# Performance work log

Measured on AMD Instinct MI355X. Metric: run time of the kernel, lower is better.

The kernel has to match this reference:

```python
import jax, jax.numpy as jnp
import numpy as np
from jax import lax

B, T, DE, DT = 64, 511, 400, 100
D = DE + DT              # encoder + tag embedding concat
S = T + 1                # head sentinel prepended
HG, HE, M = 384, 64, 32  # graph hidden, edge hidden, band width


def lstm_layer(x, h0, c0, Wih, Whh, bih, bhh):
    """x: [N, L, in] -> [N, L, H]; torch LSTM gate order (i, f, g, o)."""
    def step(carry, xt):
        h, c = carry
        gates = xt @ Wih.T + bih + h @ Whh.T + bhh
        i, f, g, o = jnp.split(gates, 4, axis=-1)
        c = jax.nn.sigmoid(f) * c + jax.nn.sigmoid(i) * jnp.tanh(g)
        h = jax.nn.sigmoid(o) * jnp.tanh(c)
        return (h, c), h
    _, ys = lax.scan(step, (h0, c0), jnp.swapaxes(x, 0, 1))
    return jnp.swapaxes(ys, 0, 1)


def setup_inputs() -> dict:
    key = jax.random.key(0)
    ks = jax.random.split(key, 32)
    def u(k, shape, h):
        s = 1.0 / np.sqrt(h)
        return jax.random.uniform(k, shape, jnp.float32, -s, s)
    return {
        "input": jax.random.normal(ks[0], (B, T, DE), jnp.float32),
        "tag_embeddings": jax.random.normal(ks[1], (B, T, DT), jnp.float32),
        "mask": jnp.ones((B, T), jnp.int32),
        "head_indices": jax.random.randint(ks[2], (B, T), 0, S),
        "head_sentinel": jax.random.normal(ks[3], (D,), jnp.float32),
        "bos_past": jnp.zeros((1,), jnp.float32),
        # graph LSTM (2 layers, dropout inactive at eval)
        "g_Wih0": u(ks[4], (4 * HG, D), HG),  "g_Whh0": u(ks[5], (4 * HG, HG), HG),
        "g_bih0": u(ks[6], (4 * HG,), HG),     "g_bhh0": u(ks[7], (4 * HG,), HG),
        "g_Wih1": u(ks[8], (4 * HG, HG), HG),  "g_Whh1": u(ks[9], (4 * HG, HG), HG),
        "g_bih1": u(ks[10], (4 * HG,), HG),    "g_bhh1": u(ks[11], (4 * HG,), HG),
        # edge LSTM past (2 layers, input size 1)
        "e_Wih0": u(ks[12], (4 * HE, 1), HE),  "e_Whh0": u(ks[13], (4 * HE, HE), HE),
        "e_bih0": u(ks[14], (4 * HE,), HE),    "e_bhh0": u(ks[15], (4 * HE,), HE),
        "e_Wih1": u(ks[16], (4 * HE, HE), HE), "e_Whh1": u(ks[17], (4 * HE, HE), HE),
        "e_bih1": u(ks[18], (4 * HE,), HE),    "e_bhh1": u(ks[19], (4 * HE,), HE),
        "g2e_W": u(ks[20], (HE, HG), HG),      "g2e_b": u(ks[21], (HE,), HG),
        "cls_W": u(ks[22], (1, HE), HE),       "cls_b": u(ks[23], (1,), HE),
        "ht_W": u(ks[24], (DT, HG), HG),       "ht_b": u(ks[25], (DT,), HG),
        "dt_W": u(ks[26], (DT, HG), HG),       "dt_b": u(ks[27], (DT,), HG),
    }


def reference(input, tag_embeddings, mask, head_indices, head_sentinel, bos_past,
              g_Wih0, g_Whh0, g_bih0, g_bhh0, g_Wih1, g_Whh1, g_bih1, g_bhh1,
              e_Wih0, e_Whh0, e_bih0, e_bhh0, e_Wih1, e_Whh1, e_bih1, e_bhh1,
              g2e_W, g2e_b, cls_W, cls_b, ht_W, ht_b, dt_W, dt_b):
    # --- sentinel prepend + adjust_for_sentinel ---
    x = jnp.concatenate([input, tag_embeddings], axis=-1)                      # [B,T,D]
    x = jnp.concatenate([jnp.broadcast_to(head_sentinel, (B, 1, D)), x], 1)    # [B,S,D]
    mask_s = jnp.concatenate([jnp.ones((B, 1), mask.dtype), mask], axis=1)
    heads = jnp.concatenate([jnp.zeros((B, 1), head_indices.dtype), head_indices], axis=1)
    # --- packed graph LSTM (2 layers, zero init); pad_packed zeros masked positions ---
    zg = jnp.zeros((B, HG), x.dtype)
    h = lstm_layer(x, zg, zg, g_Wih0, g_Whh0, g_bih0, g_bhh0)
    graph_state = lstm_layer(h, zg, zg, g_Wih1, g_Whh1, g_bih1, g_bhh1)        # [B,S,HG]
    graph_state = graph_state * mask_s[..., None].astype(graph_state.dtype)
    # --- edge_pass_train (split=False): teacher-forced banded edge LSTM ---
    proj = graph_state.reshape(B * S, HG) @ g2e_W.T + g2e_b                    # [B*S,HE]
    Lm = min(M, S)
    A_sq = jax.nn.one_hot(heads, S, dtype=jnp.float32)                         # adj_indices_to_adj_matrix
    A_in = A_sq[:, :, :Lm].reshape(B * S, Lm, 1)                               # make_adj_sequence band
    bos = jnp.broadcast_to(bos_past.reshape(1, 1, 1), (B * S, 1, 1))
    A_in = jnp.concatenate([bos, A_in], axis=1)                                # [B*S,Lm+1,1]
    ze = jnp.zeros((B * S, HE), proj.dtype)
    e = lstm_layer(A_in, proj, ze, e_Wih0, e_Whh0, e_bih0, e_bhh0)             # h0=proj per layer, c0=0
    e = lstm_layer(e, proj, ze, e_Wih1, e_Whh1, e_bih1, e_bhh1)
    edge_logits = e @ cls_W.T + cls_b                                          # [B*S,Lm+1,1]
    Ap = edge_logits[:, 1:, 0].reshape(B, S, Lm)                               # drop bos step
    # banded writeback: arc_logits[:, i, :min(S,M)] = Ap[:, i, :] for every i
    arc_logits = jnp.zeros((B, S, S), graph_state.dtype).at[:, :, :Lm].set(Ap)
    # --- tag feedforwards (dropout = identity at eval) ---
    head_tag = jax.nn.elu(graph_state @ ht_W.T + ht_b)
    dep_tag = jax.nn.elu(graph_state @ dt_W.T + dt_b)
    return arc_logits, head_tag, dep_tag
```

## Files before the change

kernel.cpp:

```cpp
#include <hip/hip_runtime.h>
#include <hip/hip_bf16.h>
#include <stdint.h>

#define BB   64
#define TT   511
#define SS   512
#define DD   500
#define KXP  512
#define HG   384
#define G4   1536
#define HE   64
#define E4   256
#define NSEQ (BB*SS)

typedef __hip_bfloat16 bf16;
typedef float  floatx4 __attribute__((ext_vector_type(4)));
typedef int    intx4   __attribute__((ext_vector_type(4)));
typedef __bf16 bfrag8  __attribute__((ext_vector_type(8)));
typedef unsigned short ushort8 __attribute__((ext_vector_type(8)));

static __device__ __forceinline__ floatx4 MFMA16(bfrag8 a, bfrag8 b, floatx4 c){
  return __builtin_amdgcn_mfma_f32_16x16x32_bf16(a, b, c, 0, 0, 0);
}
static __device__ __forceinline__ float sigm_(float x){ return 1.f/(1.f + __expf(-x)); }
static __device__ __forceinline__ float tanh_(float x){
  x = fminf(fmaxf(x, -15.f), 15.f);
  float e = __expf(2.f*x);
  return (e - 1.f)/(e + 1.f);
}
static __device__ __forceinline__ float actv(float x, bool isg){
  float s = 1.f/(1.f + __expf(isg ? -2.f*x : -x));
  return isg ? (2.f*s - 1.f) : s;
}
static __device__ __forceinline__ float b2f(unsigned short u){
  union { unsigned int i; float f; } x; x.i = ((unsigned int)u)<<16; return x.f;
}
static __device__ __forceinline__ unsigned short f2bu(float f){
  bf16 b = __float2bfloat16(f);
  return *reinterpret_cast<unsigned short*>(&b);
}
static __device__ __forceinline__ bfrag8 asfrag(intx4 v){
  union { intx4 i; bfrag8 f; } u; u.i = v; return u.f;
}

static __device__ __forceinline__ bfrag8 ldfrag_coh(const bf16* p){
  unsigned long long u0 = __hip_atomic_load((const unsigned long long*)p,     __ATOMIC_RELAXED, __HIP_MEMORY_SCOPE_SYSTEM);
  unsigned long long u1 = __hip_atomic_load((const unsigned long long*)p + 1, __ATOMIC_RELAXED, __HIP_MEMORY_SCOPE_SYSTEM);
  union { unsigned long long u[2]; bfrag8 f; } x; x.u[0]=u0; x.u[1]=u1;
  return x.f;
}
static __device__ __forceinline__ void stpair_coh(bf16* p, float lo, float hi){
  unsigned int pk = (unsigned int)f2bu(lo) | ((unsigned int)f2bu(hi) << 16);
  __hip_atomic_store((unsigned int*)p, pk, __ATOMIC_RELAXED, __HIP_MEMORY_SCOPE_SYSTEM);
}

__global__ __launch_bounds__(256) void prep_x(const float* __restrict__ input,
    const float* __restrict__ tag, const float* __restrict__ sent,
    bf16* __restrict__ Xb)
{
  const size_t N8 = (size_t)NSEQ*KXP/8;
  const size_t stp = (size_t)gridDim.x * blockDim.x;
  for (size_t i8 = (size_t)blockIdx.x*blockDim.x + threadIdx.x; i8 < N8; i8 += stp){
    int m = (int)(i8 >> 6);
    int k = ((int)i8 & 63) * 8;
    int b = m >> 9, s = m & 511;
    float v[8];
    if (s == 0){
      #pragma unroll
      for (int j=0;j<8;++j) v[j] = (k+j < DD) ? sent[k+j] : 0.f;
    } else if (k < 400){
      const float* src = input + (size_t)(b*TT + s-1)*400 + k;
      float4 a = *(const float4*)src;
      float4 c = *(const float4*)(src+4);
      v[0]=a.x; v[1]=a.y; v[2]=a.z; v[3]=a.w; v[4]=c.x; v[5]=c.y; v[6]=c.z; v[7]=c.w;
    } else if (k < 496){
      const float* src = tag + (size_t)(b*TT + s-1)*100 + (k-400);
      float4 a = *(const float4*)src;
      float4 c = *(const float4*)(src+4);
      v[0]=a.x; v[1]=a.y; v[2]=a.z; v[3]=a.w; v[4]=c.x; v[5]=c.y; v[6]=c.z; v[7]=c.w;
    } else if (k == 496){
      const float* src = tag + (size_t)(b*TT + s-1)*100 + 96;
      float4 a = *(const float4*)src;
      v[0]=a.x; v[1]=a.y; v[2]=a.z; v[3]=a.w; v[4]=0.f; v[5]=0.f; v[6]=0.f; v[7]=0.f;
    } else {
      #pragma unroll
      for (int j=0;j<8;++j) v[j]=0.f;
    }
    ushort8 o;
    #pragma unroll
    for (int j=0;j<8;++j) o[j] = f2bu(v[j]);
    *(ushort8*)&Xb[i8*8] = o;
  }
}

__global__ __launch_bounds__(256) void prep_w(
  const float* __restrict__ gWih0, const float* __restrict__ gWhh0,
  const float* __restrict__ gbih0, const float* __restrict__ gbhh0,
  const float* __restrict__ gWih1, const float* __restrict__ gWhh1,
  const float* __restrict__ gbih1, const float* __restrict__ gbhh1,
  const float* __restrict__ eWih0, const float* __restrict__ eWhh0,
  const float* __restrict__ ebih0, const float* __restrict__ ebhh0,
  const float* __restrict__ eWih1, const float* __restrict__ eWhh1,
  const float* __restrict__ ebih1, const float* __restrict__ ebhh1,
  const float* __restrict__ g2eW, const float* __restrict__ htW, const float* __restrict__ dtW,
  bf16* __restrict__ W0i, bf16* __restrict__ W0r, bf16* __restrict__ W1c,
  float* __restrict__ gb0, float* __restrict__ gb1,
  bf16* __restrict__ eW0b, bf16* __restrict__ eW1ab, bf16* __restrict__ eW1bb,
  float* __restrict__ eb0, float* __restrict__ eb1, float* __restrict__ ew0cv,
  bf16* __restrict__ g2eWb, bf16* __restrict__ htWb, bf16* __restrict__ dtWb)
{
  const int st = blockIdx.x*blockDim.x + threadIdx.x;
  const int gs = gridDim.x*blockDim.x;
  auto cvt4 = [](const float* s)->ushort4 {
    float4 f = *(const float4*)s;
    ushort4 u; u.x=f2bu(f.x); u.y=f2bu(f.y); u.z=f2bu(f.z); u.w=f2bu(f.w); return u;
  };
  for (int i4=st; i4<G4*KXP/4; i4+=gs){ int n=i4>>7, kk=(i4&127)*4; int j=n>>2, g=n&3;
      ushort4 u;
      if (kk < DD) u = cvt4(&gWih0[(size_t)(g*HG+j)*DD + kk]);
      else { u.x=u.y=u.z=u.w=0; }
      *(ushort4*)&W0i[(size_t)i4*4] = u; }
  for (int i4=st; i4<G4*HG/4; i4+=gs){ int n=i4/96, kk=(i4%96)*4; int j=n>>2, g=n&3;
      *(ushort4*)&W0r[(size_t)i4*4] = cvt4(&gWhh0[(size_t)(g*HG+j)*HG + kk]); }
  for (int i4=st; i4<G4*768/4; i4+=gs){ int n=i4/192, kk=(i4%192)*4; int j=n>>2, g=n&3;
      const float* s = (kk<HG) ? &gWih1[(size_t)(g*HG+j)*HG + kk]
                               : &gWhh1[(size_t)(g*HG+j)*HG + (kk-HG)];
      *(ushort4*)&W1c[(size_t)i4*4] = cvt4(s); }
  for (int i=st; i<G4; i+=gs){ int j=i>>2, g=i&3; int s=g*HG+j;
      gb0[i]=gbih0[s]+gbhh0[s]; gb1[i]=gbih1[s]+gbhh1[s]; }
  for (int i4=st; i4<E4*HE/4; i4+=gs){
      *(ushort4*)&eW0b [(size_t)i4*4] = cvt4(&eWhh0[(size_t)i4*4]);
      *(ushort4*)&eW1ab[(size_t)i4*4] = cvt4(&eWih1[(size_t)i4*4]);
      *(ushort4*)&eW1bb[(size_t)i4*4] = cvt4(&eWhh1[(size_t)i4*4]); }
  for (int i=st; i<E4; i+=gs){ eb0[i]=ebih0[i]+ebhh0[i]; eb1[i]=ebih1[i]+ebhh1[i];
      ew0cv[i]=eWih0[i]; }
  for (int i4=st; i4<HE*HG/4; i4+=gs)
      *(ushort4*)&g2eWb[(size_t)i4*4] = cvt4(&g2eW[(size_t)i4*4]);
  for (int i4=st; i4<128*HG/4; i4+=gs){ int i=i4*4;
      ushort4 uh, ud;
      if (i < 100*HG){ uh = cvt4(&htW[i]); ud = cvt4(&dtW[i]); }
      else { uh.x=uh.y=uh.z=uh.w=0; ud=uh; }
      *(ushort4*)&htWb[i] = uh; *(ushort4*)&dtWb[i] = ud; }
}

template<int KTOT,int BN,int WAVES_M,int WAVES_N,int EPI>
__device__ __forceinline__ void gemm_body(int bid,
    const bf16* __restrict__ A, const bf16* __restrict__ Wt,
    const float* __restrict__ bias, const int* __restrict__ mask,
    void* __restrict__ outp, int Nreal)
{
  constexpr int WMT = 128/(WAVES_M*16);
  constexpr int WNT = BN /(WAVES_N*16);
  __shared__ alignas(16) bf16 As[128][32];
  __shared__ alignas(16) bf16 Bs[BN][32];
  const int tid = threadIdx.x;
  const int bm = bid & 255, bn = bid >> 8;
  const int m0 = bm*128, n0 = bn*BN;
  const int wid = tid>>6, l = tid&63, lj = l&15, lq = l>>4;
  const int wm = wid / WAVES_N, wn = wid % WAVES_N;
  floatx4 acc[WMT][WNT] = {};
  for (int k0 = 0; k0 < KTOT; k0 += 32){
    __syncthreads();
    for (int c = tid; c < 128*4; c += 256){
      int row = c>>2, ch = c&3;
      *(uint4*)&As[row][ch*8] = *(const uint4*)&A[(size_t)(m0+row)*KTOT + k0 + ch*8];
    }
    for (int c = tid; c < BN*4; c += 256){
      int row = c>>2, ch = c&3;
      *(uint4*)&Bs[row][ch*8] = *(const uint4*)&Wt[(size_t)(n0+row)*KTOT + k0 + ch*8];
    }
    __syncthreads();
    bfrag8 af[WMT]; bfrag8 bfr[WNT];
    #pragma unroll
    for (int mi=0;mi<WMT;++mi) af[mi]  = *(const bfrag8*)&As[wm*WMT*16 + mi*16 + lj][lq*8];
    #pragma unroll
    for (int ni=0;ni<WNT;++ni) bfr[ni] = *(const bfrag8*)&Bs[wn*WNT*16 + ni*16 + lj][lq*8];
    #pragma unroll
    for (int mi=0;mi<WMT;++mi)
      #pragma unroll
      for (int ni=0;ni<WNT;++ni)
        acc[mi][ni] = MFMA16(af[mi], bfr[ni], acc[mi][ni]);
  }
  #pragma unroll
  for (int mi=0;mi<WMT;++mi){
    #pragma unroll
    for (int ni=0;ni<WNT;++ni){
      #pragma unroll
      for (int r=0;r<4;++r){
        int grow = m0 + wm*WMT*16 + mi*16 + 4*lq + r;
        int gcol = n0 + wn*WNT*16 + ni*16 + lj;
        float v = acc[mi][ni][r];
        if (EPI == 3){
          v += bias[gcol];
          int s = grow & 511, b = grow >> 9;
          ((bf16*)outp)[((size_t)s*BB + b)*G4 + gcol] = __float2bfloat16(v);
        } else {
          int s = grow & 511, b = grow >> 9;
          float mk = (s==0) ? 1.f : (float)mask[b*TT + s - 1];
          v = v*mk + bias[gcol];
          if (EPI == 1){
            ((bf16*)outp)[(size_t)grow*Nreal + gcol] = __float2bfloat16(v);
          } else {
            v = v > 0.f ? v : expm1f(v);
            if (gcol < Nreal) ((float*)outp)[(size_t)grow*Nreal + gcol] = v;
          }
        }
      }
    }
  }
}

__global__ __launch_bounds__(256) void gemm_g0(
    const bf16* __restrict__ Xb, const bf16* __restrict__ W0i,
    const float* __restrict__ gb0, bf16* __restrict__ G0t)
{
  gemm_body<KXP,128,2,2,3>(blockIdx.x, Xb, W0i, gb0, nullptr, (void*)G0t, G4);
}

__global__ __launch_bounds__(256) void gemm_proj(
    const bf16* __restrict__ h1seq, const bf16* __restrict__ g2eWb,
    const float* __restrict__ g2eb, const int* __restrict__ mask,
    bf16* __restrict__ projb)
{
  gemm_body<HG,64,4,1,1>(blockIdx.x, h1seq, g2eWb, g2eb, mask, (void*)projb, HE);
}

template<int IS1>
__device__ __forceinline__ void rnn_body(int bid, int tid,
    const bf16* __restrict__ G0t, const bf16* __restrict__ Wsrc,
    const float* __restrict__ gb1,
    bf16* __restrict__ h0seq, bf16* __restrict__ h1seq, unsigned int* __restrict__ flags)
{
  constexpr int KW = IS1 ? 768 : 384;
  constexpr int KF = IS1 ? 24 : 12;
  const int bl = IS1 ? bid-48 : bid;
  const int w = tid>>6, l = tid&63, lj = l&15, lq = l>>4;
  const int m0 = w*16;
  const int n0 = bl*32;
  const int a  = lj>>2;
  const int gl = l&3;
  const bool isg = (gl==2);

  intx4 Wr0[KF], Wr1[KF];
  #pragma unroll
  for (int kf=0; kf<KF; ++kf){
    Wr0[kf] = *(const intx4*)&Wsrc[(size_t)(n0 + lj)*KW      + kf*32 + lq*8];
    Wr1[kf] = *(const intx4*)&Wsrc[(size_t)(n0 + 16 + lj)*KW + kf*32 + lq*8];
  }
  #pragma unroll
  for (int kf=0; kf<KF; ++kf)
    asm volatile("" : "+v"(Wr0[kf]), "+v"(Wr1[kf]));

  float bi0 = 0.f, bi1 = 0.f;
  if (IS1){ bi0 = gb1[n0 + 4*a + gl]; bi1 = gb1[n0 + 16 + 4*a + gl]; }

  float c0s[4]={0,0,0,0}, c1s[4]={0,0,0,0};
  unsigned short g0pre[2][4];
  if (!IS1){
    #pragma unroll
    for (int nt=0;nt<2;++nt)
      #pragma unroll
      for (int r=0;r<4;++r)
        g0pre[nt][r] = *(const unsigned short*)&G0t[(size_t)(m0 + 4*lq + r)*G4 + n0 + nt*16 + 4*a + gl];
  }
  unsigned int* myflag = flags + (size_t)(((IS1?48:0) + bl)*4 + w)*16;
  unsigned int* f0p = flags + (size_t)((l)*4 + w)*16;
  unsigned int* f1p = flags + (size_t)((48 + l)*4 + w)*16;

  const int ITMAX = IS1 ? SS : (SS-1);
  for (int it=0; it<=ITMAX; ++it){
    if (it >= 1){
      const unsigned tgt = (unsigned)it;
      const bool need = (l < 48);
      while (true){
        bool ok = true;
        if (need){
          unsigned f0 = __hip_atomic_load(f0p, __ATOMIC_RELAXED, __HIP_MEMORY_SCOPE_AGENT);
          ok = (f0 >= tgt);
          if (IS1){
            unsigned f1 = __hip_atomic_load(f1p, __ATOMIC_RELAXED, __HIP_MEMORY_SCOPE_AGENT);
            ok = ok && (f1 >= tgt);
          }
        }
        if (__all(ok)) break;
        __builtin_amdgcn_s_sleep(1);
      }
      asm volatile("" ::: "memory");
    }
    if (!IS1 || it >= 1){
      const int t = IS1 ? it-1 : it;
      bfrag8 ha[KF];
      if (IS1){
        const bf16* hb0 = h0seq + ((size_t)t*BB + (m0+lj))*HG;
        #pragma unroll
        for (int kf=0;kf<12;++kf) ha[kf] = ldfrag_coh(hb0 + kf*32 + lq*8);
        if (t > 0){
          const bf16* hb1 = h1seq + ((size_t)(m0+lj)*SS + (t-1))*HG;
          #pragma unroll
          for (int kf=12;kf<24;++kf) ha[kf] = ldfrag_coh(hb1 + (kf-12)*32 + lq*8);
        }
      } else if (t > 0){
        const bf16* hb = h0seq + ((size_t)(t-1)*BB + (m0+lj))*HG;
        #pragma unroll
        for (int kf=0;kf<12;++kf) ha[kf] = ldfrag_coh(hb + kf*32 + lq*8);
      }
      floatx4 aA0={0,0,0,0}, aB0={0,0,0,0}, aA1={0,0,0,0}, aB1={0,0,0,0};
      if (IS1 || t > 0){
        #pragma unroll
        for (int kf=0;kf<12;++kf){
          if (kf&1){ aB0 = MFMA16(ha[kf], asfrag(Wr0[kf]), aB0); aB1 = MFMA16(ha[kf], asfrag(Wr1[kf]), aB1); }
          else     { aA0 = MFMA16(ha[kf], asfrag(Wr0[kf]), aA0); aA1 = MFMA16(ha[kf], asfrag(Wr1[kf]), aA1); }
        }
      }
      if (IS1 && t > 0){
        #pragma unroll
        for (int kf=12;kf<24;++kf){
          if (kf&1){ aB0 = MFMA16(ha[kf], asfrag(Wr0[kf]), aB0); aB1 = MFMA16(ha[kf], asfrag(Wr1[kf]), aB1); }
          else     { aA0 = MFMA16(ha[kf], asfrag(Wr0[kf]), aA0); aA1 = MFMA16(ha[kf], asfrag(Wr1[kf]), aA1); }
        }
      }
      const floatx4 s0 = aA0 + aB0, s1 = aA1 + aB1;
      #pragma unroll
      for (int nt=0; nt<2; ++nt){
        #pragma unroll
        for (int r=0; r<4; ++r){
          float x = nt ? s1[r] : s0[r];
          x += IS1 ? (nt ? bi1 : bi0) : b2f(g0pre[nt][r]);
          float av = actv(x, isg);
          float i_ = __shfl(av, (l&60)|0);
          float f_ = __shfl(av, (l&60)|1);
          float g_ = __shfl(av, (l&60)|2);
          float o_ = __shfl(av, (l&60)|3);
          float cp = nt ? c1s[r] : c0s[r];
          float c = f_*cp + i_*g_;
          if (nt) c1s[r] = c; else c0s[r] = c;
          float h = o_*tanh_(c);
          float hn = __shfl(h, l^4);
          if ((l&7) == 0){
            int bb = m0 + 4*lq + r;
            int jh = bl*8 + nt*4 + a;
            bf16* hp = IS1 ? (h1seq + ((size_t)bb*SS + t)*HG + jh)
                           : (h0seq + ((size_t)t*BB + bb)*HG + jh);
            stpair_coh(hp, h, hn);
          }
        }
      }
    }
    asm volatile("s_waitcnt vmcnt(0)" ::: "memory");
    if (l == 0)
      __hip_atomic_store(myflag, (unsigned)(it+1),
                         __ATOMIC_RELAXED, __HIP_MEMORY_SCOPE_AGENT);
    if (!IS1 && it+1 <= ITMAX){
      #pragma unroll
      for (int nt=0;nt<2;++nt)
        #pragma unroll
        for (int r=0;r<4;++r)
          g0pre[nt][r] = *(const unsigned short*)&G0t[((size_t)(it+1)*BB + m0 + 4*lq + r)*G4 + n0 + nt*16 + 4*a + gl];
    }
  }
}

__global__ __launch_bounds__(256,1) void graph_rnn(
    const bf16* __restrict__ G0t, const bf16* __restrict__ W0r, const bf16* __restrict__ W1c,
    const float* __restrict__ gb1, bf16* __restrict__ h0seq, bf16* __restrict__ h1seq,
    unsigned int* flags)
{
  if (blockIdx.x < 48) rnn_body<0>(blockIdx.x, threadIdx.x, G0t, W0r, gb1, h0seq, h1seq, flags);
  else                 rnn_body<1>(blockIdx.x, threadIdx.x, G0t, W1c, gb1, h0seq, h1seq, flags);
}

__device__ void edge_body(int bid,
    const bf16* __restrict__ projb,
    const bf16* __restrict__ eW0b, const bf16* __restrict__ eW1ab, const bf16* __restrict__ eW1bb,
    const float* __restrict__ eb0, const float* __restrict__ eb1, const float* __restrict__ ew0c,
    const float* __restrict__ clsW, const float* __restrict__ clsb_p, const float* __restrict__ bos_p,
    const int* __restrict__ heads, float* __restrict__ arc)
{
  __shared__ alignas(16) bf16 hbuf0[16][72];
  __shared__ alignas(16) bf16 hbuf1[16][72];
  __shared__ float lbuf[4][16];
  const int tid = threadIdx.x, w = tid>>6, l = tid&63, lj = l&15, lq = l>>4;
  const int seq0 = bid * 16;
  const int jglob = w*16 + lj;
  for (int i = tid; i < 16*64; i += 256){
    int sl = i >> 6, jj = i & 63;
    bf16 v = projb[(size_t)(seq0+sl)*HE + jj];
    hbuf0[sl][jj] = v; hbuf1[sl][jj] = v;
  }
  bfrag8 W0f[4][2], W1af[4][2], W1bf[4][2];
  #pragma unroll
  for (int g=0; g<4; ++g){
    #pragma unroll
    for (int kk=0; kk<2; ++kk){
      size_t offw = (size_t)(g*HE + jglob)*HE + kk*32 + lq*8;
      W0f [g][kk] = *(const bfrag8*)&eW0b [offw];
      W1af[g][kk] = *(const bfrag8*)&eW1ab[offw];
      W1bf[g][kk] = *(const bfrag8*)&eW1bb[offw];
    }
  }
  float ebr0[4], ebr1[4], ewr[4];
  #pragma unroll
  for (int g=0; g<4; ++g){ ebr0[g]=eb0[g*HE+jglob]; ebr1[g]=eb1[g*HE+jglob]; ewr[g]=ew0c[g*HE+jglob]; }
  const float clswj = clsW[jglob];
  const float bos = bos_p[0], clsb = clsb_p[0];
  int hd[4]; float c0r[4]={0,0,0,0}, c1r[4]={0,0,0,0};
  #pragma unroll
  for (int r=0;r<4;++r){
    int sq = seq0 + 4*lq + r;
    int b = sq >> 9, s = sq & 511;
    hd[r] = (s==0) ? 0 : heads[b*TT + s - 1];
  }
  __syncthreads();
  for (int j=0; j<33; ++j){
    floatx4 acc0[4] = {};
    bfrag8 a0[2];
    #pragma unroll
    for (int kk=0; kk<2; ++kk)
      a0[kk] = *(const bfrag8*)((const char*)&hbuf0[0][0] + lj*144 + kk*64 + lq*16);
    #pragma unroll
    for (int g=0; g<4; ++g)
      #pragma unroll
      for (int kk=0; kk<2; ++kk)
        acc0[g] = MFMA16(a0[kk], W0f[g][kk], acc0[g]);
    __syncthreads();
    float h0v[4];
    #pragma unroll
    for (int r=0;r<4;++r){
      float x = (j==0) ? bos : ((hd[r] == j-1) ? 1.f : 0.f);
      float pi = acc0[0][r] + ebr0[0] + x*ewr[0];
      float pf = acc0[1][r] + ebr0[1] + x*ewr[1];
      float pg = acc0[2][r] + ebr0[2] + x*ewr[2];
      float po = acc0[3][r] + ebr0[3] + x*ewr[3];
      float i_=sigm_(pi), f_=sigm_(pf), g_=tanh_(pg), o_=sigm_(po);
      c0r[r] = f_*c0r[r] + i_*g_;
      h0v[r] = o_*tanh_(c0r[r]);
    }
    #pragma unroll
    for (int r=0;r<4;++r) hbuf0[4*lq + r][jglob] = __float2bfloat16(h0v[r]);
    __syncthreads();
    floatx4 acc1[4] = {};
    bfrag8 a1[2], a2[2];
    #pragma unroll
    for (int kk=0;kk<2;++kk){
      a1[kk] = *(const bfrag8*)((const char*)&hbuf0[0][0] + lj*144 + kk*64 + lq*16);
      a2[kk] = *(const bfrag8*)((const char*)&hbuf1[0][0] + lj*144 + kk*64 + lq*16);
    }
    #pragma unroll
    for (int g=0; g<4; ++g){
      #pragma unroll
      for (int kk=0;kk<2;++kk){
        acc1[g] = MFMA16(a1[kk], W1af[g][kk], acc1[g]);
        acc1[g] = MFMA16(a2[kk], W1bf[g][kk], acc1[g]);
      }
    }
    __syncthreads();
    float p[4];
    #pragma unroll
    for (int r=0;r<4;++r){
      float pi = acc1[0][r] + ebr1[0];
      float pf = acc1[1][r] + ebr1[1];
      float pg = acc1[2][r] + ebr1[2];
      float po = acc1[3][r] + ebr1[3];
      float i_=sigm_(pi), f_=sigm_(pf), g_=tanh_(pg), o_=sigm_(po);
      c1r[r] = f_*c1r[r] + i_*g_;
      float h1 = o_*tanh_(c1r[r]);
      hbuf1[4*lq + r][jglob] = __float2bfloat16(h1);
      p[r] = h1 * clswj;
    }
    #pragma unroll
    for (int mk=1; mk<16; mk<<=1)
      #pragma unroll
      for (int r=0;r<4;++r) p[r] += __shfl_xor(p[r], mk, 64);
    if (lj == 0){
      #pragma unroll
      for (int r=0;r<4;++r) lbuf[w][4*lq + r] = p[r];
    }
    __syncthreads();
    if (tid < 16 && j >= 1){
      int sq = seq0 + tid;
      float v = lbuf[0][tid] + lbuf[1][tid] + lbuf[2][tid] + lbuf[3][tid] + clsb;
      arc[(size_t)sq*SS + (j-1)] = v;
    }
  }
}

__global__ __launch_bounds__(256) void edge_tag(
    const bf16* __restrict__ projb,
    const bf16* __restrict__ eW0b, const bf16* __restrict__ eW1ab, const bf16* __restrict__ eW1bb,
    const float* __restrict__ eb0, const float* __restrict__ eb1, const float* __restrict__ ew0c,
    const float* __restrict__ clsW, const float* __restrict__ clsb_p, const float* __restrict__ bos_p,
    const int* __restrict__ heads, float* __restrict__ arc,
    const bf16* __restrict__ h1seq,
    const bf16* __restrict__ htWb, const float* __restrict__ htb,
    const bf16* __restrict__ dtWb, const float* __restrict__ dtb,
    const int* __restrict__ mask, float* __restrict__ out_ht, float* __restrict__ out_dt)
{
  const int b = blockIdx.x;
  if (b < 2048)      edge_body(b, projb, eW0b, eW1ab, eW1bb, eb0, eb1, ew0c,
                               clsW, clsb_p, bos_p, heads, arc);
  else if (b < 2304) gemm_body<HG,128,2,2,2>(b-2048, h1seq, htWb, htb, mask, (void*)out_ht, 100);
  else               gemm_body<HG,128,2,2,2>(b-2304, h1seq, dtWb, dtb, mask, (void*)out_dt, 100);
}

extern "C" void kernel_launch(void* const* d_in, const int* in_sizes, int n_in,
                              void* d_out, int out_size, void* d_ws, size_t ws_size,
                              hipStream_t stream)
{
  const float* input = (const float*)d_in[0];
  const float* tag   = (const float*)d_in[1];
  const int*   mask  = (const int*)  d_in[2];
  const int*   heads = (const int*)  d_in[3];
  const float* sent  = (const float*)d_in[4];
  const float* bosp  = (const float*)d_in[5];
  const float* gWih0 = (const float*)d_in[6];
  const float* gWhh0 = (const float*)d_in[7];
  const float* gbih0 = (const float*)d_in[8];
  const float* gbhh0 = (const float*)d_in[9];
  const float* gWih1 = (const float*)d_in[10];
  const float* gWhh1 = (const float*)d_in[11];
  const float* gbih1 = (const float*)d_in[12];
  const float* gbhh1 = (const float*)d_in[13];
  const float* eWih0 = (const float*)d_in[14];
  const float* eWhh0 = (const float*)d_in[15];
  const float* ebih0 = (const float*)d_in[16];
  const float* ebhh0 = (const float*)d_in[17];
  const float* eWih1 = (const float*)d_in[18];
  const float* eWhh1 = (const float*)d_in[19];
  const float* ebih1 = (const float*)d_in[20];
  const float* ebhh1 = (const float*)d_in[21];
  const float* g2eW  = (const float*)d_in[22];
  const float* g2eb  = (const float*)d_in[23];
  const float* clsW  = (const float*)d_in[24];
  const float* clsb  = (const float*)d_in[25];
  const float* htW   = (const float*)d_in[26];
  const float* htb   = (const float*)d_in[27];
  const float* dtW   = (const float*)d_in[28];
  const float* dtb   = (const float*)d_in[29];

  char* wsb = (char*)d_ws;
  size_t off = 0;
  auto take = [&](size_t bytes)->char* {
    char* p = wsb + off;
    off = (off + bytes + 255) & ~(size_t)255;
    return p;
  };
  bf16*  Xb     = (bf16*) take((size_t)NSEQ*KXP*2);
  bf16*  W0i    = (bf16*) take((size_t)G4*KXP*2);
  bf16*  W0r    = (bf16*) take((size_t)G4*HG*2);
  bf16*  W1c    = (bf16*) take((size_t)G4*768*2);
  float* gb0i   = (float*)take(G4*4);
  float* gb1i   = (float*)take(G4*4);
  bf16*  G0t    = (bf16*) take((size_t)NSEQ*G4*2);
  bf16*  h0seq  = (bf16*) take((size_t)SS*BB*HG*2);
  bf16*  h1seq  = (bf16*) take((size_t)NSEQ*HG*2);
  unsigned int* flags = (unsigned int*)take(384*16*4);
  bf16*  projb  = (bf16*) take((size_t)NSEQ*HE*2);
  bf16*  eW0b   = (bf16*) take(E4*HE*2);
  bf16*  eW1ab  = (bf16*) take(E4*HE*2);
  bf16*  eW1bb  = (bf16*) take(E4*HE*2);
  float* eb0w   = (float*)take(E4*4);
  float* eb1w   = (float*)take(E4*4);
  float* ew0cw  = (float*)take(E4*4);
  bf16*  g2eWb  = (bf16*) take(HE*HG*2);
  bf16*  htWb   = (bf16*) take(128*HG*2);
  bf16*  dtWb   = (bf16*) take(128*HG*2);

  (void)hipMemsetAsync(d_out, 0, (size_t)16777216*4, stream);
  (void)hipMemsetAsync(flags, 0, 384*16*4, stream);

  prep_x<<<2048,256,0,stream>>>(input, tag, sent, Xb);
  prep_w<<<512,256,0,stream>>>(gWih0,gWhh0,gbih0,gbhh0,gWih1,gWhh1,gbih1,gbhh1,
                               eWih0,eWhh0,ebih0,ebhh0,eWih1,eWhh1,ebih1,ebhh1,
                               g2eW,htW,dtW,
                               W0i,W0r,W1c,gb0i,gb1i,eW0b,eW1ab,eW1bb,
                               eb0w,eb1w,ew0cw,g2eWb,htWb,dtWb);

  gemm_g0<<<3072,256,0,stream>>>(Xb, W0i, gb0i, G0t);

  graph_rnn<<<96,256,0,stream>>>(G0t, W0r, W1c, gb1i, h0seq, h1seq, flags);

  gemm_proj<<<256,256,0,stream>>>(h1seq, g2eWb, g2eb, mask, projb);

  edge_tag<<<2560,256,0,stream>>>(projb, eW0b, eW1ab, eW1bb, eb0w, eb1w, ew0cw,
                                  clsW, clsb, bosp, heads, (float*)d_out,
                                  h1seq, htWb, htb, dtWb, dtb, mask,
                                  (float*)d_out + 16777216,
                                  (float*)d_out + 16777216 + 3276800);
}
```

Measured before the change: 4.859 ms.

## Poison-fill hidden-state buffers and validate loads instead of waiting on stores before flag

Fills h0seq/h1seq with a NaN-pattern poison value in prep_w. Consumers in the persistent graph RNN re-poll any fragment that still holds the poison after the flag wait. This lets the producer drop the s_waitcnt vmcnt(0) before publishing its step flag, so the store latency is meant to come off the serial recurrence critical path. It adds a large memset-like fill and retry loops, and it depends on real h values never equalling the poison pair.

```diff
diff --git a/kernel.cpp b/kernel.cpp
--- a/kernel.cpp
+++ b/kernel.cpp
@@ -12,6 +12,7 @@
 #define HE   64
 #define E4   256
 #define NSEQ (BB*SS)
+#define POISON32 0x7FC07FC0u
 
 typedef __hip_bfloat16 bf16;
 typedef float  floatx4 __attribute__((ext_vector_type(4)));
@@ -43,15 +44,59 @@
   union { intx4 i; bfrag8 f; } u; u.i = v; return u.f;
 }
 
-static __device__ __forceinline__ bfrag8 ldfrag_coh(const bf16* p){
+static __device__ __forceinline__ intx4 ld16_chk(const bf16* p){
   unsigned long long u0 = __hip_atomic_load((const unsigned long long*)p,     __ATOMIC_RELAXED, __HIP_MEMORY_SCOPE_SYSTEM);
   unsigned long long u1 = __hip_atomic_load((const unsigned long long*)p + 1, __ATOMIC_RELAXED, __HIP_MEMORY_SCOPE_SYSTEM);
-  union { unsigned long long u[2]; bfrag8 f; } x; x.u[0]=u0; x.u[1]=u1;
-  return x.f;
+  union { unsigned long long u[2]; intx4 v; } x; x.u[0]=u0; x.u[1]=u1;
+  return x.v;
+}
+static __device__ __forceinline__ bool okfrag(intx4 v){
+  return (((unsigned)v.x) != POISON32) & (((unsigned)v.y) != POISON32) &
+         (((unsigned)v.z) != POISON32) & (((unsigned)v.w) != POISON32);
 }
 static __device__ __forceinline__ void stpair_coh(bf16* p, float lo, float hi){
   unsigned int pk = (unsigned int)f2bu(lo) | ((unsigned int)f2bu(hi) << 16);
   __hip_atomic_store((unsigned int*)p, pk, __ATOMIC_RELAXED, __HIP_MEMORY_SCOPE_SYSTEM);
+}
+template<int NF>
+static __device__ __forceinline__ void loadN_chk(const bf16* base, int lq, intx4* ha){
+  #pragma unroll
+  for (int kf=0;kf<NF;++kf) ha[kf] = ld16_chk(base + kf*32 + lq*8);
+  unsigned okm = 0;
+  #pragma unroll
+  for (int kf=0;kf<NF;++kf) if (okfrag(ha[kf])) okm |= (1u<<kf);
+  const unsigned FULL = (1u<<NF)-1u;
+  while (!__all(okm == FULL)){
+    __builtin_amdgcn_s_sleep(1);
+    #pragma unroll
+    for (int kf=0;kf<NF;++kf){
+      if (!(okm & (1u<<kf))){
+        ha[kf] = ld16_chk(base + kf*32 + lq*8);
+        if (okfrag(ha[kf])) okm |= (1u<<kf);
+      }
+    }
+  }
+}
+static __device__ __forceinline__ void load24_chk(const bf16* b0, const bf16* b1, int lq, intx4* ha){
+  #pragma unroll
+  for (int kf=0;kf<24;++kf){
+    const bf16* p = (kf<12) ? (b0 + kf*32 + lq*8) : (b1 + (kf-12)*32 + lq*8);
+    ha[kf] = ld16_chk(p);
+  }
+  unsigned okm = 0;
+  #pragma unroll
+  for (int kf=0;kf<24;++kf) if (okfrag(ha[kf])) okm |= (1u<<kf);
+  while (!__all(okm == 0xFFFFFFu)){
+    __builtin_amdgcn_s_sleep(1);
+    #pragma unroll
+    for (int kf=0;kf<24;++kf){
+      if (!(okm & (1u<<kf))){
+        const bf16* p = (kf<12) ? (b0 + kf*32 + lq*8) : (b1 + (kf-12)*32 + lq*8);
+        ha[kf] = ld16_chk(p);
+        if (okfrag(ha[kf])) okm |= (1u<<kf);
+      }
+    }
+  }
 }
 
 __global__ __launch_bounds__(256) void prep_x(const float* __restrict__ input,
@@ -107,7 +152,8 @@
   float* __restrict__ gb0, float* __restrict__ gb1,
   bf16* __restrict__ eW0b, bf16* __restrict__ eW1ab, bf16* __restrict__ eW1bb,
   float* __restrict__ eb0, float* __restrict__ eb1, float* __restrict__ ew0cv,
-  bf16* __restrict__ g2eWb, bf16* __restrict__ htWb, bf16* __restrict__ dtWb)
+  bf16* __restrict__ g2eWb, bf16* __restrict__ htWb, bf16* __restrict__ dtWb,
+  unsigned int* __restrict__ h0_u, unsigned int* __restrict__ h1_u)
 {
   const int st = blockIdx.x*blockDim.x + threadIdx.x;
   const int gs = gridDim.x*blockDim.x;
@@ -141,6 +187,8 @@
       if (i < 100*HG){ uh = cvt4(&htW[i]); ud = cvt4(&dtW[i]); }
       else { uh.x=uh.y=uh.z=uh.w=0; ud=uh; }
       *(ushort4*)&htWb[i] = uh; *(ushort4*)&dtWb[i] = ud; }
+  for (int i=st; i<SS*BB*HG/2; i+=gs) h0_u[i] = POISON32;
+  for (int i=st; i<NSEQ*HG/2;  i+=gs) h1_u[i] = POISON32;
 }
 
 template<int KTOT,int BN,int WAVES_M,int WAVES_N,int EPI>
@@ -289,34 +337,32 @@
     }
     if (!IS1 || it >= 1){
       const int t = IS1 ? it-1 : it;
-      bfrag8 ha[KF];
+      intx4 ha[KF];
       if (IS1){
         const bf16* hb0 = h0seq + ((size_t)t*BB + (m0+lj))*HG;
-        #pragma unroll
-        for (int kf=0;kf<12;++kf) ha[kf] = ldfrag_coh(hb0 + kf*32 + lq*8);
         if (t > 0){
           const bf16* hb1 = h1seq + ((size_t)(m0+lj)*SS + (t-1))*HG;
-          #pragma unroll
-          for (int kf=12;kf<24;++kf) ha[kf] = ldfrag_coh(hb1 + (kf-12)*32 + lq*8);
+          load24_chk(hb0, hb1, lq, ha);
+        } else {
+          loadN_chk<12>(hb0, lq, ha);
         }
       } else if (t > 0){
         const bf16* hb = h0seq + ((size_t)(t-1)*BB + (m0+lj))*HG;
-        #pragma unroll
-        for (int kf=0;kf<12;++kf) ha[kf] = ldfrag_coh(hb + kf*32 + lq*8);
+        loadN_chk<12>(hb, lq, ha);
       }
       floatx4 aA0={0,0,0,0}, aB0={0,0,0,0}, aA1={0,0,0,0}, aB1={0,0,0,0};
       if (IS1 || t > 0){
         #pragma unroll
         for (int kf=0;kf<12;++kf){
-          if (kf&1){ aB0 = MFMA16(ha[kf], asfrag(Wr0[kf]), aB0); aB1 = MFMA16(ha[kf], asfrag(Wr1[kf]), aB1); }
-          else     { aA0 = MFMA16(ha[kf], asfrag(Wr0[kf]), aA0); aA1 = MFMA16(ha[kf], asfrag(Wr1[kf]), aA1); }
+          if (kf&1){ aB0 = MFMA16(asfrag(ha[kf]), asfrag(Wr0[kf]), aB0); aB1 = MFMA16(asfrag(ha[kf]), asfrag(Wr1[kf]), aB1); }
+          else     { aA0 = MFMA16(asfrag(ha[kf]), asfrag(Wr0[kf]), aA0); aA1 = MFMA16(asfrag(ha[kf]), asfrag(Wr1[kf]), aA1); }
         }
       }
       if (IS1 && t > 0){
         #pragma unroll
         for (int kf=12;kf<24;++kf){
-          if (kf&1){ aB0 = MFMA16(ha[kf], asfrag(Wr0[kf]), aB0); aB1 = MFMA16(ha[kf], asfrag(Wr1[kf]), aB1); }
-          else     { aA0 = MFMA16(ha[kf], asfrag(Wr0[kf]), aA0); aA1 = MFMA16(ha[kf], asfrag(Wr1[kf]), aA1); }
+          if (kf&1){ aB0 = MFMA16(asfrag(ha[kf]), asfrag(Wr0[kf]), aB0); aB1 = MFMA16(asfrag(ha[kf]), asfrag(Wr1[kf]), aB1); }
+          else     { aA0 = MFMA16(asfrag(ha[kf]), asfrag(Wr0[kf]), aA0); aA1 = MFMA16(asfrag(ha[kf]), asfrag(Wr1[kf]), aA1); }
         }
       }
       const floatx4 s0 = aA0 + aB0, s1 = aA1 + aB1;
@@ -346,7 +392,8 @@
         }
       }
     }
-    asm volatile("s_waitcnt vmcnt(0)" ::: "memory");
+    __builtin_amdgcn_sched_barrier(0);
+    asm volatile("" ::: "memory");
     if (l == 0)
       __hip_atomic_store(myflag, (unsigned)(it+1),
                          __ATOMIC_RELAXED, __HIP_MEMORY_SCOPE_AGENT);
@@ -573,7 +620,8 @@
                                eWih0,eWhh0,ebih0,ebhh0,eWih1,eWhh1,ebih1,ebhh1,
                                g2eW,htW,dtW,
                                W0i,W0r,W1c,gb0i,gb1i,eW0b,eW1ab,eW1bb,
-                               eb0w,eb1w,ew0cw,g2eWb,htWb,dtWb);
+                               eb0w,eb1w,ew0cw,g2eWb,htWb,dtWb,
+                               (unsigned int*)h0seq, (unsigned int*)h1seq);
 
   gemm_g0<<<3072,256,0,stream>>>(Xb, W0i, gb0i, G0t);
 
```

New measurement: 4.921 ms. About the same (+1.3%).
